# Performance work log

Hardware: AMD Instinct MI355X
Metric: run time of the kernel (lower is better)

Reference implementation:

```python
import jax, jax.numpy as jnp
import numpy as np

MARGIN = 0.2  # matches init_kwargs; margin > 0 -> relu hinge branch

N_PARTS, NUM_CLASSES, K_PER_CLASS, D_FEAT = 64, 32, 16, 256


def setup_inputs() -> dict:
    key = jax.random.key(0)
    m = NUM_CLASSES * K_PER_CLASS  # 512
    feature = jax.random.normal(key, (N_PARTS, m, D_FEAT), dtype=jnp.float32)
    # Structured P x K labels: masked_select(...).view(n, m, -1, 1) in the
    # original requires exactly K positives per anchor, so labels must be
    # K samples per class (identical across the part dimension).
    label = jnp.tile(jnp.repeat(jnp.arange(NUM_CLASSES, dtype=jnp.int64), K_PER_CLASS)[None, :], (N_PARTS, 1))
    return {"feature": feature, "label": label, "num_pos": K_PER_CLASS}


def _batch_euc_dist(x):
    # x: [n, m, d] -> dist: [n, m, m]
    x2 = jnp.sum(x * x, axis=2)  # [n, m]
    d2 = x2[:, :, None] + x2[:, None, :] - 2.0 * jnp.einsum('nid,njd->nij', x, x)
    return jnp.sqrt(jax.nn.relu(d2))


def reference(feature, label, num_pos):
    n, m, d = feature.shape
    dist = _batch_euc_dist(feature)  # [n, m, m]
    same = label[:, :, None] == label[:, None, :]  # [n, m, m] bool
    # masked_select preserves flat (row-major) order, so per anchor the
    # selected positives/negatives appear in increasing index order ->
    # stable argsort on the mask reproduces it exactly.
    pos_idx = jnp.argsort(jnp.where(same, 0, 1), axis=-1)[..., :num_pos]        # [n, m, k]
    neg_idx = jnp.argsort(jnp.where(same, 1, 0), axis=-1)[..., :m - num_pos]    # [n, m, m-k]
    hp = jnp.take_along_axis(dist, pos_idx, axis=-1)[:, :, :, None]   # [n, m, k, 1]
    hn = jnp.take_along_axis(dist, neg_idx, axis=-1)[:, :, None, :]   # [n, m, 1, m-k]
    # margin > 0 -> relu hinge (heter/hard/part mining disabled by init flags)
    loss = jax.nn.relu(MARGIN + hp - hn).reshape(n, -1)               # [n, m*k*(m-k)]
    nonzero_num = jnp.sum(loss != 0, axis=1).astype(loss.dtype)       # [n]
    loss_mean = jnp.where(nonzero_num == 0, 0.0,
                          jnp.sum(loss, axis=1) / jnp.maximum(nonzero_num, 1.0))
    return loss_mean.mean(), nonzero_num.mean()
```

## Files before the change

### kernel.cpp

```cpp
#include <hip/hip_runtime.h>
#include <math.h>


#define MARGIN 0.2f
constexpr int NP = 64;
constexpr int M = 512;
constexpr int D = 256;
constexpr int SDS = 20;

typedef __attribute__((ext_vector_type(8))) short bf16x8;
typedef __attribute__((ext_vector_type(4))) float f32x4;

__device__ __forceinline__ unsigned f2bf(float x) {
  unsigned b = __float_as_uint(x);
  return (b + 0x7FFFu + ((b >> 16) & 1u)) >> 16;
}
__device__ __forceinline__ uint4 pack8u(float4 v0, float4 v1) {
  uint4 p;
  p.x = f2bf(v0.x) | (f2bf(v0.y) << 16);
  p.y = f2bf(v0.z) | (f2bf(v0.w) << 16);
  p.z = f2bf(v1.x) | (f2bf(v1.y) << 16);
  p.w = f2bf(v1.z) | (f2bf(v1.w) << 16);
  return p;
}
__device__ __forceinline__ bf16x8 pack8b(float4 v0, float4 v1) {
  union { uint4 u; bf16x8 b; } cv;
  cv.u = pack8u(v0, v1);
  return cv.b;
}
__device__ __forceinline__ float sq8(float4 v0, float4 v1) {
  return v0.x * v0.x + v0.y * v0.y + v0.z * v0.z + v0.w * v0.w +
         v1.x * v1.x + v1.y * v1.y + v1.z * v1.z + v1.w * v1.w;
}

__global__ __launch_bounds__(256, 2) void triplet_kernel(
    const float* __restrict__ feat, float* __restrict__ psum,
    float* __restrict__ pcnt) {
  __shared__ unsigned short Bs[64 * 16 * 8];
  __shared__ float sortd[64 * SDS];
  __shared__ float sumt[64 * SDS];
  __shared__ float x2s[64];
  __shared__ float reds[4], redc[4];

  const int p = blockIdx.x;
  const int diag = blockIdx.y;
  const int h = blockIdx.z;
  const int i0 = diag * 64;
  const int t = threadIdx.x;
  const int w = t >> 6, L = t & 63;
  const int tx = L & 15, quad = L >> 4;
  const int br = t >> 4, bc = t & 15;

  const float* fp = feat + (size_t)p * M * D;

  bf16x8 af[8];
#pragma unroll
  for (int kc = 0; kc < 2; kc++)
#pragma unroll
    for (int ks = 0; ks < 4; ks++) {
      const float* src =
          fp + (size_t)(i0 + w * 16 + tx) * D + kc * 128 + (ks * 4 + quad) * 8;
      af[kc * 4 + ks] = pack8b(((const float4*)src)[0], ((const float4*)src)[1]);
    }

  float x2i[4];
  f32x4 srt[4][4];
  float hsum = 0.f;
  int hcnt = 0;

  const int ntiles = 4 + h;
  for (int ti = 0; ti < ntiles; ti++) {
    const int tt = (ti == 0) ? 0 : ti + h * 3;
    const int j0 = ((diag + tt) & 7) * 64;
    f32x4 acc[4];
#pragma unroll
    for (int f = 0; f < 4; f++) acc[f] = (f32x4){0.f, 0.f, 0.f, 0.f};
    float rowss[4];

#pragma unroll
    for (int kc = 0; kc < 2; kc++) {
      __syncthreads();
#pragma unroll
      for (int r4 = 0; r4 < 4; r4++) {
        const int row = br + r4 * 16;
        const float* src = fp + (size_t)(j0 + row) * D + kc * 128 + bc * 8;
        float4 v0 = ((const float4*)src)[0], v1 = ((const float4*)src)[1];
        *(uint4*)&Bs[(row * 16 + (bc ^ (row & 7))) * 8] = pack8u(v0, v1);
        const float s8 = sq8(v0, v1);
        rowss[r4] = kc ? rowss[r4] + s8 : s8;
      }
      if (kc == 1) {
#pragma unroll
        for (int r4 = 0; r4 < 4; r4++) {
          float ss = rowss[r4];
          ss += __shfl_xor(ss, 8, 16);
          ss += __shfl_xor(ss, 4, 16);
          ss += __shfl_xor(ss, 2, 16);
          ss += __shfl_xor(ss, 1, 16);
          if (bc == 0) x2s[br + r4 * 16] = ss;
        }
      }
      __syncthreads();
#pragma unroll
      for (int ks = 0; ks < 4; ks++) {
        const bf16x8 a = af[kc * 4 + ks];
#pragma unroll
        for (int f = 0; f < 4; f++) {
          const int rowb = f * 16 + tx, cb = ks * 4 + quad;
          bf16x8 b = *(bf16x8*)&Bs[(rowb * 16 + (cb ^ (rowb & 7))) * 8];
          acc[f] =
              __builtin_amdgcn_mfma_f32_16x16x32_bf16(a, b, acc[f], 0, 0, 0);
        }
      }
    }

    if (ti == 0) {
#pragma unroll
      for (int r = 0; r < 4; r++) x2i[r] = x2s[w * 16 + quad * 4 + r];
      const float xj = x2s[w * 16 + tx];
#pragma unroll
      for (int r = 0; r < 4; r++) {
        float d2 = x2i[r] + xj - 2.f * acc[w][r];
        sortd[(w * 16 + quad * 4 + r) * SDS + tx] =
            MARGIN + sqrtf(fmaxf(d2, 0.f));
      }
      __syncthreads();
      if (t < 64) {
        float v[16];
#pragma unroll
        for (int q4 = 0; q4 < 4; q4++) {
          f32x4 vv = *(f32x4*)&sortd[t * SDS + q4 * 4];
          v[q4 * 4 + 0] = vv.x; v[q4 * 4 + 1] = vv.y;
          v[q4 * 4 + 2] = vv.z; v[q4 * 4 + 3] = vv.w;
        }
#pragma unroll
        for (int k = 2; k <= 16; k <<= 1)
#pragma unroll
          for (int j = k >> 1; j > 0; j >>= 1)
#pragma unroll
            for (int i = 0; i < 16; i++) {
              const int l = i ^ j;
              if (l > i) {
                const bool asc = ((i & k) == 0);
                if (asc ? (v[i] > v[l]) : (v[i] < v[l])) {
                  float tmp = v[i]; v[i] = v[l]; v[l] = tmp;
                }
              }
            }
#pragma unroll
        for (int q4 = 0; q4 < 4; q4++)
          *(f32x4*)&sortd[t * SDS + q4 * 4] =
              (f32x4){v[q4 * 4], v[q4 * 4 + 1], v[q4 * 4 + 2], v[q4 * 4 + 3]};
        float run = 0.f;
        sumt[t * SDS + 0] = 0.f;
#pragma unroll
        for (int c = 1; c <= 16; c++) {
          run += v[16 - c];
          sumt[t * SDS + c] = run;
        }
      }
      __syncthreads();
#pragma unroll
      for (int r = 0; r < 4; r++)
#pragma unroll
        for (int q4 = 0; q4 < 4; q4++)
          srt[r][q4] = *(f32x4*)&sortd[(w * 16 + quad * 4 + r) * SDS + q4 * 4];

      if (h == 0) {
#pragma unroll
        for (int f = 0; f < 4; f++) {
          if (f == w) continue;
          const float xj2 = x2s[f * 16 + tx];
#pragma unroll
          for (int r = 0; r < 4; r++) {
            const float dn = sqrtf(fmaxf(x2i[r] + xj2 - 2.f * acc[f][r], 0.f));
            int c = 0;
#define CMP(sv) c += ((sv) > dn) ? 1 : 0;
            CMP(srt[r][0].x) CMP(srt[r][0].y) CMP(srt[r][0].z) CMP(srt[r][0].w)
            CMP(srt[r][1].x) CMP(srt[r][1].y) CMP(srt[r][1].z) CMP(srt[r][1].w)
            CMP(srt[r][2].x) CMP(srt[r][2].y) CMP(srt[r][2].z) CMP(srt[r][2].w)
            CMP(srt[r][3].x) CMP(srt[r][3].y) CMP(srt[r][3].z) CMP(srt[r][3].w)
#undef CMP
            hsum += sumt[(w * 16 + quad * 4 + r) * SDS + c];
            hsum = fmaf(-(float)c, dn, hsum);
            hcnt += c;
          }
        }
      }
    } else {
#pragma unroll
      for (int f = 0; f < 4; f++) {
        const float xj = x2s[f * 16 + tx];
#pragma unroll
        for (int r = 0; r < 4; r++) {
          const float dn = sqrtf(fmaxf(x2i[r] + xj - 2.f * acc[f][r], 0.f));
          int c = 0;
#define CMP(sv) c += ((sv) > dn) ? 1 : 0;
          CMP(srt[r][0].x) CMP(srt[r][0].y) CMP(srt[r][0].z) CMP(srt[r][0].w)
          CMP(srt[r][1].x) CMP(srt[r][1].y) CMP(srt[r][1].z) CMP(srt[r][1].w)
          CMP(srt[r][2].x) CMP(srt[r][2].y) CMP(srt[r][2].z) CMP(srt[r][2].w)
          CMP(srt[r][3].x) CMP(srt[r][3].y) CMP(srt[r][3].z) CMP(srt[r][3].w)
#undef CMP
          hsum += sumt[(w * 16 + quad * 4 + r) * SDS + c];
          hsum = fmaf(-(float)c, dn, hsum);
          hcnt += c;
        }
      }
    }
  }

  float cf = (float)hcnt;
  for (int off = 32; off > 0; off >>= 1) {
    hsum += __shfl_down(hsum, off, 64);
    cf += __shfl_down(cf, off, 64);
  }
  if (L == 0) { reds[w] = hsum; redc[w] = cf; }
  __syncthreads();
  if (t == 0) {
    psum[p * 16 + diag * 2 + h] = reds[0] + reds[1] + reds[2] + reds[3];
    pcnt[p * 16 + diag * 2 + h] = redc[0] + redc[1] + redc[2] + redc[3];
  }
}

__global__ __launch_bounds__(64) void finalize_kernel(
    const float* __restrict__ psum, const float* __restrict__ pcnt,
    float* __restrict__ out) {
  const int p = threadIdx.x;
  float s = 0.f, c = 0.f;
#pragma unroll
  for (int i = 0; i < 16; i++) {
    s += psum[p * 16 + i];
    c += pcnt[p * 16 + i];
  }
  float lm = (c == 0.f) ? 0.f : s / fmaxf(c, 1.f);
  float ctot = c;
  for (int off = 32; off > 0; off >>= 1) {
    lm += __shfl_down(lm, off, 64);
    ctot += __shfl_down(ctot, off, 64);
  }
  if (p == 0) {
    out[0] = lm / 64.f;
    out[1] = ctot / 64.f;
  }
}

extern "C" void kernel_launch(void* const* d_in, const int* in_sizes, int n_in,
                              void* d_out, int out_size, void* d_ws,
                              size_t ws_size, hipStream_t stream) {
  const float* feat = (const float*)d_in[0];
  float* ws = (float*)d_ws;
  float* psum = ws;
  float* pcnt = ws + 1024;
  float* out = (float*)d_out;

  dim3 grid(NP, 8, 2);
  triplet_kernel<<<grid, 256, 0, stream>>>(feat, psum, pcnt);
  finalize_kernel<<<1, 64, 0, stream>>>(psum, pcnt, out);
}
```

Measured before the change: 131.6 us.

## Precompute bf16 features and norms once, stream tiles via direct global-to-LDS loads

Adds a pre-pass kernel that converts the fp32 features to a pre-swizzled bf16 buffer and computes per-row squared norms once, instead of every block re-reading fp32 and re-converting each B tile. The main kernel then loads whole 64x256 bf16 tiles straight into LDS with global_load_lds, using one sync pair per tile instead of two, and reads norms from global memory. In exchange it adds an extra kernel launch, a workspace round trip of the bf16 copy, and doubles the LDS B buffer.

```diff
diff --git a/kernel.cpp b/kernel.cpp
--- a/kernel.cpp
+++ b/kernel.cpp
@@ -10,6 +10,8 @@
 
 typedef __attribute__((ext_vector_type(8))) short bf16x8;
 typedef __attribute__((ext_vector_type(4))) float f32x4;
+typedef __attribute__((address_space(1))) const unsigned int as1_uint;
+typedef __attribute__((address_space(3))) unsigned int as3_uint;
 
 __device__ __forceinline__ unsigned f2bf(float x) {
   unsigned b = __float_as_uint(x);
@@ -23,20 +25,34 @@
   p.w = f2bf(v1.z) | (f2bf(v1.w) << 16);
   return p;
 }
-__device__ __forceinline__ bf16x8 pack8b(float4 v0, float4 v1) {
-  union { uint4 u; bf16x8 b; } cv;
-  cv.u = pack8u(v0, v1);
-  return cv.b;
-}
 __device__ __forceinline__ float sq8(float4 v0, float4 v1) {
   return v0.x * v0.x + v0.y * v0.y + v0.z * v0.z + v0.w * v0.w +
          v1.x * v1.x + v1.y * v1.y + v1.z * v1.z + v1.w * v1.w;
 }
 
+__global__ __launch_bounds__(256) void convert_kernel(
+    const float* __restrict__ feat, unsigned short* __restrict__ fb,
+    float* __restrict__ x2g) {
+  const int t = threadIdx.x;
+  const int R = blockIdx.x * 8 + (t >> 5);
+  const int c = t & 31;
+  const int r = R & 63;
+  const float* src = feat + (size_t)R * D + c * 8;
+  float4 v0 = ((const float4*)src)[0], v1 = ((const float4*)src)[1];
+  *(uint4*)&fb[((size_t)R * 32 + (c ^ (r & 7))) * 8] = pack8u(v0, v1);
+  float ss = sq8(v0, v1);
+  ss += __shfl_xor(ss, 16, 32);
+  ss += __shfl_xor(ss, 8, 32);
+  ss += __shfl_xor(ss, 4, 32);
+  ss += __shfl_xor(ss, 2, 32);
+  ss += __shfl_xor(ss, 1, 32);
+  if (c == 0) x2g[R] = ss;
+}
+
 __global__ __launch_bounds__(256, 2) void triplet_kernel(
-    const float* __restrict__ feat, float* __restrict__ psum,
-    float* __restrict__ pcnt) {
-  __shared__ unsigned short Bs[64 * 16 * 8];
+    const unsigned short* __restrict__ fb, const float* __restrict__ x2g,
+    float* __restrict__ psum, float* __restrict__ pcnt) {
+  __shared__ unsigned short Bs[64 * 32 * 8];
   __shared__ float sortd[64 * SDS];
   __shared__ float sumt[64 * SDS];
   __shared__ float x2s[64];
@@ -49,21 +65,23 @@
   const int t = threadIdx.x;
   const int w = t >> 6, L = t & 63;
   const int tx = L & 15, quad = L >> 4;
-  const int br = t >> 4, bc = t & 15;
-
-  const float* fp = feat + (size_t)p * M * D;
-
+  const int tx7 = tx & 7;
+
+  const size_t Ra = (size_t)p * M + i0 + w * 16 + tx;
   bf16x8 af[8];
 #pragma unroll
   for (int kc = 0; kc < 2; kc++)
 #pragma unroll
     for (int ks = 0; ks < 4; ks++) {
-      const float* src =
-          fp + (size_t)(i0 + w * 16 + tx) * D + kc * 128 + (ks * 4 + quad) * 8;
-      af[kc * 4 + ks] = pack8b(((const float4*)src)[0], ((const float4*)src)[1]);
+      const int ca = kc * 16 + ks * 4 + quad;
+      af[kc * 4 + ks] = *(const bf16x8*)&fb[(Ra * 32 + (ca ^ tx7)) * 8];
     }
 
   float x2i[4];
+#pragma unroll
+  for (int r = 0; r < 4; r++)
+    x2i[r] = x2g[(size_t)p * M + i0 + w * 16 + quad * 4 + r];
+
   f32x4 srt[4][4];
   float hsum = 0.f;
   int hcnt = 0;
@@ -72,51 +90,39 @@
   for (int ti = 0; ti < ntiles; ti++) {
     const int tt = (ti == 0) ? 0 : ti + h * 3;
     const int j0 = ((diag + tt) & 7) * 64;
+
+    __syncthreads();
+    {
+      const char* gsrc = (const char*)fb + ((size_t)p * M + j0) * 512;
+      char* lbase = (char*)Bs + (t >> 6) * 1024;
+#pragma unroll
+      for (int i = 0; i < 8; i++)
+        __builtin_amdgcn_global_load_lds(
+            (as1_uint*)(gsrc + i * 4096 + t * 16),
+            (as3_uint*)(lbase + i * 4096), 16, 0, 0);
+      if (t < 64) x2s[t] = x2g[(size_t)p * M + j0 + t];
+    }
+    __syncthreads();
+
     f32x4 acc[4];
 #pragma unroll
     for (int f = 0; f < 4; f++) acc[f] = (f32x4){0.f, 0.f, 0.f, 0.f};
-    float rowss[4];
-
-#pragma unroll
-    for (int kc = 0; kc < 2; kc++) {
-      __syncthreads();
-#pragma unroll
-      for (int r4 = 0; r4 < 4; r4++) {
-        const int row = br + r4 * 16;
-        const float* src = fp + (size_t)(j0 + row) * D + kc * 128 + bc * 8;
-        float4 v0 = ((const float4*)src)[0], v1 = ((const float4*)src)[1];
-        *(uint4*)&Bs[(row * 16 + (bc ^ (row & 7))) * 8] = pack8u(v0, v1);
-        const float s8 = sq8(v0, v1);
-        rowss[r4] = kc ? rowss[r4] + s8 : s8;
-      }
-      if (kc == 1) {
-#pragma unroll
-        for (int r4 = 0; r4 < 4; r4++) {
-          float ss = rowss[r4];
-          ss += __shfl_xor(ss, 8, 16);
-          ss += __shfl_xor(ss, 4, 16);
-          ss += __shfl_xor(ss, 2, 16);
-          ss += __shfl_xor(ss, 1, 16);
-          if (bc == 0) x2s[br + r4 * 16] = ss;
-        }
-      }
-      __syncthreads();
+#pragma unroll
+    for (int kc = 0; kc < 2; kc++)
 #pragma unroll
       for (int ks = 0; ks < 4; ks++) {
         const bf16x8 a = af[kc * 4 + ks];
+        const int cb = kc * 16 + ks * 4 + quad;
 #pragma unroll
         for (int f = 0; f < 4; f++) {
-          const int rowb = f * 16 + tx, cb = ks * 4 + quad;
-          bf16x8 b = *(bf16x8*)&Bs[(rowb * 16 + (cb ^ (rowb & 7))) * 8];
+          const int rowb = f * 16 + tx;
+          bf16x8 b = *(bf16x8*)&Bs[(rowb * 32 + (cb ^ tx7)) * 8];
           acc[f] =
               __builtin_amdgcn_mfma_f32_16x16x32_bf16(a, b, acc[f], 0, 0, 0);
         }
       }
-    }
 
     if (ti == 0) {
-#pragma unroll
-      for (int r = 0; r < 4; r++) x2i[r] = x2s[w * 16 + quad * 4 + r];
       const float xj = x2s[w * 16 + tx];
 #pragma unroll
       for (int r = 0; r < 4; r++) {
@@ -251,9 +257,12 @@
   float* ws = (float*)d_ws;
   float* psum = ws;
   float* pcnt = ws + 1024;
+  float* x2g = ws + 2048;
+  unsigned short* fb = (unsigned short*)(ws + 2048 + 32768);
   float* out = (float*)d_out;
 
+  convert_kernel<<<(NP * M) / 8, 256, 0, stream>>>(feat, fb, x2g);
   dim3 grid(NP, 8, 2);
-  triplet_kernel<<<grid, 256, 0, stream>>>(feat, psum, pcnt);
+  triplet_kernel<<<grid, 256, 0, stream>>>(fb, x2g, psum, pcnt);
   finalize_kernel<<<1, 64, 0, stream>>>(psum, pcnt, out);
 }
```

Measured after the change: 123.3 us. 1.07x faster.
